# Kernel tuning notes

Hardware: AMD Instinct MI355X
Metric: run time of the kernel (lower is better)

Reference implementation:

```python
import jax, jax.numpy as jnp
import numpy as np

FILTER_SIZE = 1024
NUM_HEADS = 16
D_HEAD = FILTER_SIZE // NUM_HEADS
LN_EPS = 1e-5


def setup_inputs() -> dict:
    key = jax.random.key(0)
    ks = jax.random.split(key, 10)
    B, T, D = 2, 2048, FILTER_SIZE
    s = 1.0 / np.sqrt(D)
    return {
        "x": jax.random.normal(ks[0], (B, T, D), dtype=jnp.float32),
        "Wq": jax.random.normal(ks[1], (D, D), dtype=jnp.float32) * s,
        "bq": jnp.zeros((D,), dtype=jnp.float32),
        "Wk": jax.random.normal(ks[2], (D, D), dtype=jnp.float32) * s,
        "bk": jnp.zeros((D,), dtype=jnp.float32),
        "Wv": jax.random.normal(ks[3], (D, D), dtype=jnp.float32) * s,
        "bv": jnp.zeros((D,), dtype=jnp.float32),
        "Wo": jax.random.normal(ks[4], (D, D), dtype=jnp.float32) * s,
        "bo": jnp.zeros((D,), dtype=jnp.float32),
        "gamma": jnp.ones((D,), dtype=jnp.float32),
        "beta": jnp.zeros((D,), dtype=jnp.float32),
    }


def reference(x, Wq, bq, Wk, bk, Wv, bv, Wo, bo, gamma, beta):
    B, T, D = x.shape
    H, Dh = NUM_HEADS, D_HEAD
    # Note: source splits features as (d_head, heads) with heads LAST.
    q = (x @ Wq.T + bq).reshape(B, T, Dh, H)
    k = (x @ Wk.T + bk).reshape(B, T, Dh, H)
    v = (x @ Wv.T + bv).reshape(B, T, Dh, H)
    scale = 1.0 / np.sqrt(Dh).astype(np.float32)
    # scores: (B, H, T, T)
    scores = jnp.einsum("bidh,bjdh->bhij", q, k) * scale
    attn = jax.nn.softmax(scores, axis=-1)  # dropout is identity in eval
    out = jnp.einsum("bhij,bjdh->bidh", attn, v)  # (B, T, Dh, H)
    out = out.reshape(B, T, D)  # matches permute(0,2,3,1).reshape in torch
    out = out @ Wo.T + bo
    out = out + x
    mu = jnp.mean(out, axis=-1, keepdims=True)
    var = jnp.var(out, axis=-1, keepdims=True)
    out = (out - mu) * jax.lax.rsqrt(var + LN_EPS) * gamma + beta
    return out
```

## Files before the change

### kernel.cpp

```cpp
#include <hip/hip_runtime.h>
#include <stdint.h>

#define T_SEQ 2048
#define D_MODEL 1024
#define NH 16
#define DH 64
#define NROWS 4096

typedef __bf16 bf16x8 __attribute__((ext_vector_type(8)));
typedef float floatx4 __attribute__((ext_vector_type(4)));
typedef short short4v __attribute__((ext_vector_type(4)));
typedef short short8v __attribute__((ext_vector_type(8)));

#define AS1 __attribute__((address_space(1)))
#define AS3 __attribute__((address_space(3)))

static __device__ __forceinline__ void gl2lds16(const unsigned short* g, unsigned short* s) {
    __builtin_amdgcn_global_load_lds((const AS1 unsigned int*)g, (AS3 unsigned int*)s, 16, 0, 0);
}

static __device__ __forceinline__ unsigned short f32_bf16(float f) {
    union { float f; unsigned int u; } c; c.f = f;
    unsigned int u = c.u;
    u = u + 0x7FFFu + ((u >> 16) & 1u);
    return (unsigned short)(u >> 16);
}

static __device__ __forceinline__ unsigned int pack2_bf16(float a, float b) {
    return (unsigned int)f32_bf16(a) | ((unsigned int)f32_bf16(b) << 16);
}

static __device__ __forceinline__ floatx4 mfma16(bf16x8 a, bf16x8 b, floatx4 c) {
    return __builtin_amdgcn_mfma_f32_16x16x32_bf16(a, b, c, 0, 0, 0);
}

static __device__ __forceinline__ floatx4 mfma16k16(short4v a, short4v b, floatx4 c) {
#if defined(__HIP_DEVICE_COMPILE__)
    return __builtin_amdgcn_mfma_f32_16x16x16bf16_1k(a, b, c, 0, 0, 0);
#else
    (void)a; (void)b;
    return c;
#endif
}

#define QSCALE 0.1803368801111204f
#define EXP2_SHIFT 10.0f
#define WAITCNT_VM4 0x0F74
#define WAITCNT_VM0 0x0F70

__global__ __launch_bounds__(256) void k_conv_all(const float* __restrict__ x,
                                                  const float* __restrict__ Wq,
                                                  const float* __restrict__ Wk,
                                                  const float* __restrict__ Wv,
                                                  const float* __restrict__ Wo,
                                                  unsigned short* __restrict__ x_bf,
                                                  unsigned short* __restrict__ wqkv_bf,
                                                  unsigned short* __restrict__ wo_bf) {
    int b = blockIdx.x, t = threadIdx.x;
    if (b < 4096) {
        int i = b * 1024 + t * 4;
        float4 v = *(const float4*)(x + i);
        uint2 o;
        o.x = pack2_bf16(v.x, v.y);
        o.y = pack2_bf16(v.z, v.w);
        *(uint2*)(x_bf + i) = o;
    } else if (b < 7168) {
        int idx = b - 4096;
        int tensor = idx >> 10, np = idx & 1023;
        const float* src = tensor == 0 ? Wq : tensor == 1 ? Wk : Wv;
        int f = (np & 63) * 16 + (np >> 6);
        int c = t * 4;
        float4 v = *(const float4*)(src + (long)f * D_MODEL + c);
        uint2 o;
        o.x = pack2_bf16(v.x, v.y);
        o.y = pack2_bf16(v.z, v.w);
        *(uint2*)(wqkv_bf + ((long)tensor * D_MODEL + np) * D_MODEL + c) = o;
    } else {
        int n = b - 7168;
        int fp = t * 4;
        const float* row = Wo + (long)n * D_MODEL;
        unsigned short o[4];
        #pragma unroll
        for (int k = 0; k < 4; k++) {
            int f = fp + k;
            o[k] = f32_bf16(row[(f & 63) * 16 + (f >> 6)]);
        }
        *(uint2*)(wo_bf + (long)n * D_MODEL + fp) = *(const uint2*)o;
    }
}

template <int BN, int MODE>
__global__ __launch_bounds__(256) void k_gemm(const unsigned short* __restrict__ A,
                                              const unsigned short* __restrict__ W,
                                              const float* __restrict__ b0,
                                              const float* __restrict__ b1,
                                              const float* __restrict__ b2,
                                              const float* __restrict__ resid,
                                              unsigned short* __restrict__ out_bf,
                                              unsigned short* __restrict__ vtg,
                                              float* __restrict__ out_f32) {
    constexpr int NT = BN / 32;
    constexpr int NCB = BN / 32;
    __shared__ unsigned short lds_a[128 * 64];
    __shared__ unsigned short lds_b[BN * 64];
    const int tid = threadIdx.x;
    const int w = tid >> 6, l = tid & 63;
    const int lrow = l & 15, lq = l >> 4;
    const int wm = (w >> 1) * 64, wn = (w & 1) * (BN / 2);
    const int L = blockIdx.x;
    const int bx = (L & 7) * 4 + ((L >> 3) & 3);
    const int by = L >> 5;
    const long am0 = (long)bx * 128;
    const long wn0 = (long)by * BN;

    floatx4 acc[4][NT] = {};
    const int grow = l >> 3;
    const int gcol = ((l & 7) ^ grow) * 8;
    const int sw8 = (lrow & 7);

    for (int k0 = 0; k0 < D_MODEL; k0 += 64) {
        #pragma unroll
        for (int c = 0; c < 4; c++) {
            int chunk = w * 4 + c;
            gl2lds16(A + (am0 + chunk * 8 + grow) * D_MODEL + k0 + gcol,
                     lds_a + chunk * 512);
        }
        #pragma unroll
        for (int c = 0; c < NCB; c++) {
            int chunk = w * NCB + c;
            gl2lds16(W + (wn0 + chunk * 8 + grow) * D_MODEL + k0 + gcol,
                     lds_b + chunk * 512);
        }
        __syncthreads();

        bf16x8 af[4][2], bf[NT][2];
        #pragma unroll
        for (int mt = 0; mt < 4; mt++)
            #pragma unroll
            for (int ks = 0; ks < 2; ks++)
                af[mt][ks] = *(const bf16x8*)(lds_a + (wm + mt * 16 + lrow) * 64 +
                                              (((ks * 4 + lq) ^ sw8) * 8));
        #pragma unroll
        for (int nt = 0; nt < NT; nt++)
            #pragma unroll
            for (int ks = 0; ks < 2; ks++)
                bf[nt][ks] = *(const bf16x8*)(lds_b + (wn + nt * 16 + lrow) * 64 +
                                              (((ks * 4 + lq) ^ sw8) * 8));
        #pragma unroll
        for (int mt = 0; mt < 4; mt++)
            #pragma unroll
            for (int nt = 0; nt < NT; nt++)
                #pragma unroll
                for (int ks = 0; ks < 2; ks++)
                    acc[mt][nt] = mfma16(af[mt][ks], bf[nt][ks], acc[mt][nt]);
        __syncthreads();
    }

    if (MODE == 0) {
        int tensor = by >> 3;
        int nbase = (by & 7) * 128;
        const float* bias = tensor == 0 ? b0 : tensor == 1 ? b1 : b2;
        float scale = tensor == 0 ? QSCALE : 1.0f;
        if (tensor < 2) {
            unsigned short* outt = out_bf + (size_t)tensor * (32u * T_SEQ * DH);
            #pragma unroll
            for (int mt = 0; mt < 4; mt++) {
                #pragma unroll
                for (int nt = 0; nt < NT; nt++) {
                    int n = nbase + wn + nt * 16 + lrow;
                    int h = n >> 6, d = n & 63;
                    float bb = bias[d * 16 + h];
                    #pragma unroll
                    for (int r = 0; r < 4; r++) {
                        int row = (int)am0 + wm + mt * 16 + lq * 4 + r;
                        float v = (acc[mt][nt][r] + bb) * scale;
                        int b = row >> 11, i = row & 2047;
                        long idx = ((long)(b * 16 + h) * T_SEQ + i) * DH + d;
                        outt[idx] = f32_bf16(v);
                    }
                }
            }
        } else {
            int row0 = (int)am0 + wm;
            int b = row0 >> 11;
            int blk = (row0 & 2047) >> 6;
            #pragma unroll
            for (int nt = 0; nt < NT; nt++) {
                int n = nbase + wn + nt * 16 + lrow;
                int h = n >> 6, d = n & 63;
                float bb = bias[d * 16 + h];
                long base = (((long)(b * 16 + h) * 64 + d) * 32 + blk) * 64;
                #pragma unroll
                for (int mt = 0; mt < 4; mt++) {
                    uint2 o;
                    o.x = pack2_bf16(acc[mt][nt][0] + bb, acc[mt][nt][1] + bb);
                    o.y = pack2_bf16(acc[mt][nt][2] + bb, acc[mt][nt][3] + bb);
                    *(uint2*)(vtg + base + lq * 16 + mt * 4) = o;
                }
            }
        }
    } else {
        #pragma unroll
        for (int mt = 0; mt < 4; mt++) {
            #pragma unroll
            for (int nt = 0; nt < NT; nt++) {
                int n = (int)wn0 + wn + nt * 16 + lrow;
                float bb = b0[n];
                #pragma unroll
                for (int r = 0; r < 4; r++) {
                    int row = (int)am0 + wm + mt * 16 + lq * 4 + r;
                    long idx = (long)row * D_MODEL + n;
                    out_f32[idx] = acc[mt][nt][r] + bb + resid[idx];
                }
            }
        }
    }
}

__global__ __launch_bounds__(256) void k_attn(const unsigned short* __restrict__ q_ws,
                                              const unsigned short* __restrict__ k_ws,
                                              const unsigned short* __restrict__ vtg,
                                              unsigned short* __restrict__ att) {
    __shared__ unsigned short kbuf[2 * 64 * 64];
    __shared__ unsigned short vbuf[2 * 64 * 64];
    const int tid = threadIdx.x;
    const int w = tid >> 6, l = tid & 63;
    const int lrow = l & 15, lq = l >> 4;
    const int sw = lrow & 7;
    const int L = blockIdx.x;
    const int bh = (L & 7) * 4 + ((L >> 3) & 3);
    const int i0 = (L >> 5) * 128;
    const unsigned short* kh = k_ws + (long)bh * T_SEQ * DH;
    const unsigned short* vh = vtg + (long)bh * 64 * T_SEQ;

    const int rl = l >> 3;
    const int gl = ((l & 7) ^ rl) * 8;

    bf16x8 qf[2][2];
    #pragma unroll
    for (int qt = 0; qt < 2; qt++) {
        const unsigned short* qp =
            q_ws + ((long)bh * T_SEQ + i0 + w * 32 + qt * 16 + lrow) * DH + lq * 8;
        qf[qt][0] = *(const bf16x8*)qp;
        qf[qt][1] = *(const bf16x8*)(qp + 32);
    }
    floatx4 o_acc[2][4] = {};
    floatx4 l_acc[2] = {};
    const short4v ones = {0x3F80, 0x3F80, 0x3F80, 0x3F80};

    auto stage = [&](int jt, int sel) {
        unsigned short* kd = kbuf + sel * 4096 + (w * 2) * 512;
        unsigned short* vd = vbuf + sel * 4096 + (w * 2) * 512;
        #pragma unroll
        for (int c = 0; c < 2; c++) {
            int row = w * 16 + c * 8 + rl;
            gl2lds16(kh + ((long)(jt * 64 + row)) * 64 + gl, kd + c * 512);
            gl2lds16(vh + ((long)row * 32 + jt) * 64 + gl, vd + c * 512);
        }
    };

    stage(0, 0);

    for (int jt = 0; jt < T_SEQ / 64; jt++) {
        const int cur = jt & 1;
        if (jt < T_SEQ / 64 - 1) {
            stage(jt + 1, 1 - cur);
            __builtin_amdgcn_s_waitcnt(WAITCNT_VM4);
        } else {
            __builtin_amdgcn_s_waitcnt(WAITCNT_VM0);
        }
        __builtin_amdgcn_s_barrier();

        const unsigned short* kb_ = kbuf + cur * 4096;
        const unsigned short* vb_ = vbuf + cur * 4096;

        floatx4 s0[4], s1[4];
        #pragma unroll
        for (int nt = 0; nt < 4; nt++) {
            const unsigned short* kp = kb_ + (nt * 16 + lrow) * 64;
            bf16x8 ka = *(const bf16x8*)(kp + ((lq ^ sw) * 8));
            bf16x8 kb = *(const bf16x8*)(kp + (((lq + 4) ^ sw) * 8));
            floatx4 c0 = {-EXP2_SHIFT, -EXP2_SHIFT, -EXP2_SHIFT, -EXP2_SHIFT};
            floatx4 c1 = c0;
            c0 = mfma16(ka, qf[0][0], c0);
            c0 = mfma16(kb, qf[0][1], c0);
            c1 = mfma16(ka, qf[1][0], c1);
            c1 = mfma16(kb, qf[1][1], c1);
            s0[nt] = c0;
            s1[nt] = c1;
        }
        short4v pf0[4], pf1[4];
        #pragma unroll
        for (int nt = 0; nt < 4; nt++) {
            {
                float p0 = __builtin_amdgcn_exp2f(s0[nt][0]);
                float p1 = __builtin_amdgcn_exp2f(s0[nt][1]);
                float p2 = __builtin_amdgcn_exp2f(s0[nt][2]);
                float p3 = __builtin_amdgcn_exp2f(s0[nt][3]);
                uint2 pk;
                pk.x = __builtin_amdgcn_perm(__float_as_uint(p1), __float_as_uint(p0), 0x07060302);
                pk.y = __builtin_amdgcn_perm(__float_as_uint(p3), __float_as_uint(p2), 0x07060302);
                union { uint2 u; short4v s4; } cv; cv.u = pk;
                pf0[nt] = cv.s4;
                l_acc[0] = mfma16k16(ones, pf0[nt], l_acc[0]);
            }
            {
                float p0 = __builtin_amdgcn_exp2f(s1[nt][0]);
                float p1 = __builtin_amdgcn_exp2f(s1[nt][1]);
                float p2 = __builtin_amdgcn_exp2f(s1[nt][2]);
                float p3 = __builtin_amdgcn_exp2f(s1[nt][3]);
                uint2 pk;
                pk.x = __builtin_amdgcn_perm(__float_as_uint(p1), __float_as_uint(p0), 0x07060302);
                pk.y = __builtin_amdgcn_perm(__float_as_uint(p3), __float_as_uint(p2), 0x07060302);
                union { uint2 u; short4v s4; } cv; cv.u = pk;
                pf1[nt] = cv.s4;
                l_acc[1] = mfma16k16(ones, pf1[nt], l_acc[1]);
            }
        }
        #pragma unroll
        for (int dt = 0; dt < 4; dt++) {
            const unsigned short* vp = vb_ + (dt * 16 + lrow) * 64;
            short8v v01 = *(const short8v*)(vp + (((2 * lq) ^ sw) * 8));
            short8v v23 = *(const short8v*)(vp + (((2 * lq + 1) ^ sw) * 8));
            short4v va = __builtin_shufflevector(v01, v01, 0, 1, 2, 3);
            short4v vb = __builtin_shufflevector(v01, v01, 4, 5, 6, 7);
            short4v vc = __builtin_shufflevector(v23, v23, 0, 1, 2, 3);
            short4v vd = __builtin_shufflevector(v23, v23, 4, 5, 6, 7);
            o_acc[0][dt] = mfma16k16(va, pf0[0], o_acc[0][dt]);
            o_acc[0][dt] = mfma16k16(vb, pf0[1], o_acc[0][dt]);
            o_acc[0][dt] = mfma16k16(vc, pf0[2], o_acc[0][dt]);
            o_acc[0][dt] = mfma16k16(vd, pf0[3], o_acc[0][dt]);
            o_acc[1][dt] = mfma16k16(va, pf1[0], o_acc[1][dt]);
            o_acc[1][dt] = mfma16k16(vb, pf1[1], o_acc[1][dt]);
            o_acc[1][dt] = mfma16k16(vc, pf1[2], o_acc[1][dt]);
            o_acc[1][dt] = mfma16k16(vd, pf1[3], o_acc[1][dt]);
        }
        __syncthreads();
    }
    int h = bh & 15, b = bh >> 4;
    #pragma unroll
    for (int qt = 0; qt < 2; qt++) {
        float rl2 = 1.0f / l_acc[qt][0];
        int i = i0 + w * 32 + qt * 16 + lrow;
        unsigned short* orow = att + ((long)(b * T_SEQ + i)) * D_MODEL + h * 64;
        #pragma unroll
        for (int dt = 0; dt < 4; dt++) {
            uint2 o;
            o.x = pack2_bf16(o_acc[qt][dt][0] * rl2, o_acc[qt][dt][1] * rl2);
            o.y = pack2_bf16(o_acc[qt][dt][2] * rl2, o_acc[qt][dt][3] * rl2);
            *(uint2*)(orow + dt * 16 + lq * 4) = o;
        }
    }
}

__global__ __launch_bounds__(256) void k_ln(float* __restrict__ io,
                                            const float* __restrict__ gamma,
                                            const float* __restrict__ beta) {
    int row = blockIdx.x, t = threadIdx.x;
    float* p = io + (long)row * D_MODEL + t * 4;
    float4 v = *(float4*)p;
    float s = v.x + v.y + v.z + v.w;
    float ss = v.x * v.x + v.y * v.y + v.z * v.z + v.w * v.w;
    #pragma unroll
    for (int m = 1; m < 64; m <<= 1) {
        s += __shfl_xor(s, m);
        ss += __shfl_xor(ss, m);
    }
    __shared__ float red[8];
    if ((t & 63) == 0) { red[t >> 6] = s; red[4 + (t >> 6)] = ss; }
    __syncthreads();
    s = red[0] + red[1] + red[2] + red[3];
    ss = red[4] + red[5] + red[6] + red[7];
    float mu = s * (1.0f / 1024.0f);
    float var = ss * (1.0f / 1024.0f) - mu * mu;
    float rstd = rsqrtf(var + 1e-5f);
    float4 g = *(const float4*)(gamma + t * 4);
    float4 be = *(const float4*)(beta + t * 4);
    float4 o;
    o.x = (v.x - mu) * rstd * g.x + be.x;
    o.y = (v.y - mu) * rstd * g.y + be.y;
    o.z = (v.z - mu) * rstd * g.z + be.z;
    o.w = (v.w - mu) * rstd * g.w + be.w;
    *(float4*)p = o;
}

extern "C" void kernel_launch(void* const* d_in, const int* in_sizes, int n_in,
                              void* d_out, int out_size, void* d_ws, size_t ws_size,
                              hipStream_t stream) {
    const float* x = (const float*)d_in[0];
    const float* Wq = (const float*)d_in[1];
    const float* bq = (const float*)d_in[2];
    const float* Wk = (const float*)d_in[3];
    const float* bk = (const float*)d_in[4];
    const float* Wv = (const float*)d_in[5];
    const float* bv = (const float*)d_in[6];
    const float* Wo = (const float*)d_in[7];
    const float* bo = (const float*)d_in[8];
    const float* gamma = (const float*)d_in[9];
    const float* beta = (const float*)d_in[10];
    float* out = (float*)d_out;

    char* ws = (char*)d_ws;
    unsigned short* x_bf = (unsigned short*)(ws);
    unsigned short* wqkv_bf = (unsigned short*)(ws + ((size_t)8 << 20));
    unsigned short* wo_bf = (unsigned short*)(ws + ((size_t)14 << 20));
    unsigned short* qkv_ws = (unsigned short*)(ws + ((size_t)16 << 20));
    unsigned short* att = x_bf;

    unsigned short* q_ws = qkv_ws;
    unsigned short* k_ws = qkv_ws + (size_t)32 * T_SEQ * DH;
    unsigned short* vtg = qkv_ws + (size_t)64 * T_SEQ * DH;

    k_conv_all<<<8192, 256, 0, stream>>>(x, Wq, Wk, Wv, Wo, x_bf, wqkv_bf, wo_bf);

    k_gemm<128, 0><<<768, 256, 0, stream>>>(
        x_bf, wqkv_bf, bq, bk, bv, nullptr, qkv_ws, vtg, nullptr);

    k_attn<<<512, 256, 0, stream>>>(q_ws, k_ws, vtg, att);

    k_gemm<64, 1><<<512, 256, 0, stream>>>(
        att, wo_bf, bo, nullptr, nullptr, x, nullptr, nullptr, out);

    k_ln<<<NROWS, 256, 0, stream>>>(out, gamma, beta);
}
```

Measured before the change: 215.6 us.

## Split attention KV range in two and combine partial outputs

```diff
diff --git a/kernel.cpp b/kernel.cpp
--- a/kernel.cpp
+++ b/kernel.cpp
@@ -217,10 +217,13 @@
     }
 }
 
+template <int JS>
 __global__ __launch_bounds__(256) void k_attn(const unsigned short* __restrict__ q_ws,
                                               const unsigned short* __restrict__ k_ws,
                                               const unsigned short* __restrict__ vtg,
-                                              unsigned short* __restrict__ att) {
+                                              unsigned short* __restrict__ att,
+                                              unsigned short* __restrict__ opart,
+                                              float* __restrict__ lpart) {
     __shared__ unsigned short kbuf[2 * 64 * 64];
     __shared__ unsigned short vbuf[2 * 64 * 64];
     const int tid = threadIdx.x;
@@ -229,7 +232,11 @@
     const int sw = lrow & 7;
     const int L = blockIdx.x;
     const int bh = (L & 7) * 4 + ((L >> 3) & 3);
-    const int i0 = (L >> 5) * 128;
+    const int rest = L >> 5;
+    const int i0 = (JS == 1 ? rest : (rest & 15)) * 128;
+    const int s = (JS == 1 ? 0 : (rest >> 4));
+    constexpr int NTILE = (T_SEQ / 64) / JS;
+    const int jt0 = s * NTILE;
     const unsigned short* kh = k_ws + (long)bh * T_SEQ * DH;
     const unsigned short* vh = vtg + (long)bh * 64 * T_SEQ;
 
@@ -259,11 +266,12 @@
         }
     };
 
-    stage(0, 0);
-
-    for (int jt = 0; jt < T_SEQ / 64; jt++) {
-        const int cur = jt & 1;
-        if (jt < T_SEQ / 64 - 1) {
+    stage(jt0, 0);
+
+    for (int u = 0; u < NTILE; u++) {
+        const int jt = jt0 + u;
+        const int cur = u & 1;
+        if (u < NTILE - 1) {
             stage(jt + 1, 1 - cur);
             __builtin_amdgcn_s_waitcnt(WAITCNT_VM4);
         } else {
@@ -337,20 +345,68 @@
         }
         __syncthreads();
     }
+
+    if (JS == 1) {
+        int h = bh & 15, b = bh >> 4;
+        #pragma unroll
+        for (int qt = 0; qt < 2; qt++) {
+            float rl2 = 1.0f / l_acc[qt][0];
+            int i = i0 + w * 32 + qt * 16 + lrow;
+            unsigned short* orow = att + ((long)(b * T_SEQ + i)) * D_MODEL + h * 64;
+            #pragma unroll
+            for (int dt = 0; dt < 4; dt++) {
+                uint2 o;
+                o.x = pack2_bf16(o_acc[qt][dt][0] * rl2, o_acc[qt][dt][1] * rl2);
+                o.y = pack2_bf16(o_acc[qt][dt][2] * rl2, o_acc[qt][dt][3] * rl2);
+                *(uint2*)(orow + dt * 16 + lq * 4) = o;
+            }
+        }
+    } else {
+        #pragma unroll
+        for (int qt = 0; qt < 2; qt++) {
+            int i = i0 + w * 32 + qt * 16 + lrow;
+            long base = (((long)(s * 32 + bh)) * T_SEQ + i) * 64;
+            #pragma unroll
+            for (int dt = 0; dt < 4; dt++) {
+                uint2 o;
+                o.x = pack2_bf16(o_acc[qt][dt][0], o_acc[qt][dt][1]);
+                o.y = pack2_bf16(o_acc[qt][dt][2], o_acc[qt][dt][3]);
+                *(uint2*)(opart + base + dt * 16 + lq * 4) = o;
+            }
+            if (lq == 0)
+                lpart[((long)(s * 32 + bh)) * T_SEQ + i] = l_acc[qt][0];
+        }
+    }
+}
+
+__global__ __launch_bounds__(256) void k_combine(const unsigned short* __restrict__ opart,
+                                                 const float* __restrict__ lpart,
+                                                 unsigned short* __restrict__ att) {
+    int blk = blockIdx.x;
+    int bh = blk >> 6, ic = blk & 63;
+    int t = threadIdx.x;
+    int il = t >> 3, dg = (t & 7) * 8;
+    long i = (long)ic * 32 + il;
+    long base0 = (((long)bh) * T_SEQ + i) * 64 + dg;
+    long base1 = (((long)(32 + bh)) * T_SEQ + i) * 64 + dg;
+    uint4 a = *(const uint4*)(opart + base0);
+    uint4 b4 = *(const uint4*)(opart + base1);
+    float rl = 1.0f / (lpart[(long)bh * T_SEQ + i] + lpart[(long)(32 + bh) * T_SEQ + i]);
+    unsigned int ua[4] = {a.x, a.y, a.z, a.w};
+    unsigned int ub[4] = {b4.x, b4.y, b4.z, b4.w};
+    unsigned int uo[4];
+    #pragma unroll
+    for (int k = 0; k < 4; k++) {
+        float a0 = __uint_as_float((ua[k] & 0xFFFFu) << 16);
+        float a1 = __uint_as_float(ua[k] & 0xFFFF0000u);
+        float b0 = __uint_as_float((ub[k] & 0xFFFFu) << 16);
+        float b1 = __uint_as_float(ub[k] & 0xFFFF0000u);
+        uo[k] = pack2_bf16((a0 + b0) * rl, (a1 + b1) * rl);
+    }
     int h = bh & 15, b = bh >> 4;
-    #pragma unroll
-    for (int qt = 0; qt < 2; qt++) {
-        float rl2 = 1.0f / l_acc[qt][0];
-        int i = i0 + w * 32 + qt * 16 + lrow;
-        unsigned short* orow = att + ((long)(b * T_SEQ + i)) * D_MODEL + h * 64;
-        #pragma unroll
-        for (int dt = 0; dt < 4; dt++) {
-            uint2 o;
-            o.x = pack2_bf16(o_acc[qt][dt][0] * rl2, o_acc[qt][dt][1] * rl2);
-            o.y = pack2_bf16(o_acc[qt][dt][2] * rl2, o_acc[qt][dt][3] * rl2);
-            *(uint2*)(orow + dt * 16 + lq * 4) = o;
-        }
-    }
+    unsigned short* dst = att + ((long)(b * T_SEQ + i)) * D_MODEL + h * 64 + dg;
+    uint4 o; o.x = uo[0]; o.y = uo[1]; o.z = uo[2]; o.w = uo[3];
+    *(uint4*)dst = o;
 }
 
 __global__ __launch_bounds__(256) void k_ln(float* __restrict__ io,
@@ -405,18 +461,27 @@
     unsigned short* wqkv_bf = (unsigned short*)(ws + ((size_t)8 << 20));
     unsigned short* wo_bf = (unsigned short*)(ws + ((size_t)14 << 20));
     unsigned short* qkv_ws = (unsigned short*)(ws + ((size_t)16 << 20));
+    unsigned short* opart = (unsigned short*)(ws + ((size_t)40 << 20));
+    float* lpart = (float*)(ws + ((size_t)56 << 20));
     unsigned short* att = x_bf;
 
     unsigned short* q_ws = qkv_ws;
     unsigned short* k_ws = qkv_ws + (size_t)32 * T_SEQ * DH;
     unsigned short* vtg = qkv_ws + (size_t)64 * T_SEQ * DH;
 
+    const bool use_split = ws_size >= ((size_t)60 << 20);
+
     k_conv_all<<<8192, 256, 0, stream>>>(x, Wq, Wk, Wv, Wo, x_bf, wqkv_bf, wo_bf);
 
     k_gemm<128, 0><<<768, 256, 0, stream>>>(
         x_bf, wqkv_bf, bq, bk, bv, nullptr, qkv_ws, vtg, nullptr);
 
-    k_attn<<<512, 256, 0, stream>>>(q_ws, k_ws, vtg, att);
+    if (use_split) {
+        k_attn<2><<<1024, 256, 0, stream>>>(q_ws, k_ws, vtg, nullptr, opart, lpart);
+        k_combine<<<2048, 256, 0, stream>>>(opart, lpart, att);
+    } else {
+        k_attn<1><<<512, 256, 0, stream>>>(q_ws, k_ws, vtg, att, nullptr, nullptr);
+    }
 
     k_gemm<64, 1><<<512, 256, 0, stream>>>(
         att, wo_bf, bo, nullptr, nullptr, x, nullptr, nullptr, out);
```

New measurement: 222.4 us. 3.1% more time.

## Double-buffer GEMM K-loop LDS staging with async global-to-LDS prefetch

Applied to the files above, without the earlier changes.

```diff
diff --git a/kernel.cpp b/kernel.cpp
--- a/kernel.cpp
+++ b/kernel.cpp
@@ -45,8 +45,7 @@
 
 #define QSCALE 0.1803368801111204f
 #define EXP2_SHIFT 10.0f
-#define WAITCNT_VM4 0x0F74
-#define WAITCNT_VM0 0x0F70
+#define WAITCNT_VM(n) (0x0F70 | (n))
 
 __global__ __launch_bounds__(256) void k_conv_all(const float* __restrict__ x,
                                                   const float* __restrict__ Wq,
@@ -101,8 +100,9 @@
                                               float* __restrict__ out_f32) {
     constexpr int NT = BN / 32;
     constexpr int NCB = BN / 32;
-    __shared__ unsigned short lds_a[128 * 64];
-    __shared__ unsigned short lds_b[BN * 64];
+    constexpr int NDMA = 4 + NCB;
+    __shared__ unsigned short lds_a[2 * 128 * 64];
+    __shared__ unsigned short lds_b[2 * BN * 64];
     const int tid = threadIdx.x;
     const int w = tid >> 6, l = tid & 63;
     const int lrow = l & 15, lq = l >> 4;
@@ -118,33 +118,48 @@
     const int gcol = ((l & 7) ^ grow) * 8;
     const int sw8 = (lrow & 7);
 
-    for (int k0 = 0; k0 < D_MODEL; k0 += 64) {
+    auto stage = [&](int ki, int sel) {
+        unsigned short* la = lds_a + sel * 8192;
+        unsigned short* lb = lds_b + sel * (BN * 64);
+        int k0 = ki * 64;
         #pragma unroll
         for (int c = 0; c < 4; c++) {
             int chunk = w * 4 + c;
-            gl2lds16(A + (am0 + chunk * 8 + grow) * D_MODEL + k0 + gcol,
-                     lds_a + chunk * 512);
+            gl2lds16(A + (am0 + chunk * 8 + grow) * D_MODEL + k0 + gcol, la + chunk * 512);
         }
         #pragma unroll
         for (int c = 0; c < NCB; c++) {
             int chunk = w * NCB + c;
-            gl2lds16(W + (wn0 + chunk * 8 + grow) * D_MODEL + k0 + gcol,
-                     lds_b + chunk * 512);
-        }
-        __syncthreads();
-
+            gl2lds16(W + (wn0 + chunk * 8 + grow) * D_MODEL + k0 + gcol, lb + chunk * 512);
+        }
+    };
+
+    stage(0, 0);
+
+    for (int i = 0; i < 16; i++) {
+        const int cur = i & 1;
+        if (i < 15) {
+            stage(i + 1, 1 - cur);
+            __builtin_amdgcn_s_waitcnt(WAITCNT_VM(NDMA));
+        } else {
+            __builtin_amdgcn_s_waitcnt(WAITCNT_VM(0));
+        }
+        __builtin_amdgcn_s_barrier();
+
+        const unsigned short* la = lds_a + cur * 8192;
+        const unsigned short* lb = lds_b + cur * (BN * 64);
         bf16x8 af[4][2], bf[NT][2];
         #pragma unroll
         for (int mt = 0; mt < 4; mt++)
             #pragma unroll
             for (int ks = 0; ks < 2; ks++)
-                af[mt][ks] = *(const bf16x8*)(lds_a + (wm + mt * 16 + lrow) * 64 +
+                af[mt][ks] = *(const bf16x8*)(la + (wm + mt * 16 + lrow) * 64 +
                                               (((ks * 4 + lq) ^ sw8) * 8));
         #pragma unroll
         for (int nt = 0; nt < NT; nt++)
             #pragma unroll
             for (int ks = 0; ks < 2; ks++)
-                bf[nt][ks] = *(const bf16x8*)(lds_b + (wn + nt * 16 + lrow) * 64 +
+                bf[nt][ks] = *(const bf16x8*)(lb + (wn + nt * 16 + lrow) * 64 +
                                               (((ks * 4 + lq) ^ sw8) * 8));
         #pragma unroll
         for (int mt = 0; mt < 4; mt++)
@@ -153,7 +168,7 @@
                 #pragma unroll
                 for (int ks = 0; ks < 2; ks++)
                     acc[mt][nt] = mfma16(af[mt][ks], bf[nt][ks], acc[mt][nt]);
-        __syncthreads();
+        __builtin_amdgcn_s_barrier();
     }
 
     if (MODE == 0) {
@@ -261,13 +276,14 @@
 
     stage(0, 0);
 
-    for (int jt = 0; jt < T_SEQ / 64; jt++) {
+    constexpr int NTILE = T_SEQ / 64;
+    for (int jt = 0; jt < NTILE; jt++) {
         const int cur = jt & 1;
-        if (jt < T_SEQ / 64 - 1) {
+        if (jt < NTILE - 1) {
             stage(jt + 1, 1 - cur);
-            __builtin_amdgcn_s_waitcnt(WAITCNT_VM4);
+            __builtin_amdgcn_s_waitcnt(WAITCNT_VM(4));
         } else {
-            __builtin_amdgcn_s_waitcnt(WAITCNT_VM0);
+            __builtin_amdgcn_s_waitcnt(WAITCNT_VM(0));
         }
         __builtin_amdgcn_s_barrier();
 
@@ -335,7 +351,7 @@
             o_acc[1][dt] = mfma16k16(vc, pf1[2], o_acc[1][dt]);
             o_acc[1][dt] = mfma16k16(vd, pf1[3], o_acc[1][dt]);
         }
-        __syncthreads();
+        __builtin_amdgcn_s_barrier();
     }
     int h = bh & 15, b = bh >> 4;
     #pragma unroll
```

New measurement: 212.7 us. No clear change (-1.3%).
